# Kernel optimization log

Measured on AMD Instinct MI355X. Metric: run time of the kernel, lower is better.

The kernel has to match this reference:

```python
import jax, jax.numpy as jnp
import numpy as np

# decoded layout constants
NN, NO, SD = 16, 8, 4          # num_neighbors, num_obstacles, state_dim_per_agent
B = 131072                      # batch rows
H1, E, HP, AD = 64, 16, 64, 2   # phi hidden, embed, psi hidden, action dim
D_ROBOT, D_OBST = 0.3, 0.3
B_GAMMA, B_EXPH = 0.05, 1.0
PHI_MIN, PHI_MAX = -2.0, 2.0
A_MAX = 2.0


def setup_inputs() -> dict:
    key = jax.random.key(0)
    kx, kw = jax.random.split(key)
    # x: [count | goal(SD) | NN neighbor rel-states (SD each) | NO obstacle rel-pos (2 each)]
    x = jax.random.normal(kx, (B, 1 + SD + SD * NN + 2 * NO), dtype=jnp.float32) * 2.0
    x = x.at[:, 0].set(float(NN))
    names = [("Wp1n", (SD, H1)), ("bp1n", (H1,)), ("Wp2n", (H1, E)), ("bp2n", (E,)),
             ("Wr1n", (E, H1)), ("br1n", (H1,)), ("Wr2n", (H1, E)), ("br2n", (E,)),
             ("Wp1o", (2, H1)), ("bp1o", (H1,)), ("Wp2o", (H1, E)), ("bp2o", (E,)),
             ("Wr1o", (E, H1)), ("br1o", (H1,)), ("Wr2o", (H1, E)), ("br2o", (E,)),
             ("Wpsi1", (2 * E + SD, HP)), ("bpsi1", (HP,)), ("Wpsi2", (HP, AD)), ("bpsi2", (AD,))]
    ks = jax.random.split(kw, len(names))
    inp = {"x": x}
    for (n, sh), k in zip(names, ks):
        s = 1.0 / np.sqrt(sh[0])  # torch Linear default init scale
        inp[n] = jax.random.uniform(k, sh, jnp.float32, -s, s)
    return inp


def _mlp2(h, W1, b1, W2, b2):
    # Feedforward: activation between layers, linear output
    return jax.nn.relu(h @ W1 + b1) @ W2 + b2


def _deepset(el, Wp1, bp1, Wp2, bp2, Wr1, br1, Wr2, br2):
    # el: [B, n, d] -> phi each element, sum over set, rho
    phi = _mlp2(el, Wp1, bp1, Wp2, bp2)          # [B, n, E]
    return _mlp2(phi.sum(axis=1), Wr1, br1, Wr2, br2)  # [B, E]


def _barrier_sum(P, D):
    # P: [B, n, 2]; APF barrier gamma * P / (|P| * (|P|-D)^exph), summed over n
    nrm = jnp.linalg.norm(P, axis=-1, keepdims=True)   # [B, n, 1]
    H = nrm - D
    return (B_GAMMA * P / (nrm * H ** B_EXPH)).sum(axis=1)  # [B, 2]


def reference(x, Wp1n, bp1n, Wp2n, bp2n, Wr1n, br1n, Wr2n, br2n,
              Wp1o, bp1o, Wp2o, bp2o, Wr1o, br1o, Wr2o, br2o,
              Wpsi1, bpsi1, Wpsi2, bpsi2):
    nb = x.shape[0]
    g = x[:, 1:1 + SD]                                        # goal
    nbr = x[:, 1 + SD:1 + SD + SD * NN].reshape(nb, NN, SD)   # neighbor rel-states
    obs = x[:, 1 + SD + SD * NN:].reshape(nb, NO, 2)          # obstacle rel-pos

    rho_n = _deepset(nbr, Wp1n, bp1n, Wp2n, bp2n, Wr1n, br1n, Wr2n, br2n)
    rho_o = _deepset(obs, Wp1o, bp1o, Wp2o, bp2o, Wr1o, br1o, Wr2o, br2o)

    h = jnp.concatenate([rho_n, rho_o, g], axis=1)            # [B, 2E+SD]
    emp = _mlp2(h, Wpsi1, bpsi1, Wpsi2, bpsi2)                # psi network
    emp = (jnp.tanh(emp) + 1.0) / 2.0 * (PHI_MAX - PHI_MIN) + PHI_MIN  # scale_empty

    bar = _barrier_sum(-nbr[:, :, :2], D_ROBOT) + _barrier_sum(-obs, D_OBST)

    action = emp + bar
    # scale(): divide rows whose inf-norm exceeds a_max
    inv_alpha = jnp.maximum(jnp.max(jnp.abs(action), axis=1, keepdims=True) / A_MAX, 1.0)
    return action / inv_alpha
```

## Files before the change

### kernel.cpp

```cpp
#include <hip/hip_runtime.h>
#include <math.h>


typedef __attribute__((ext_vector_type(8))) _Float16 f16x8;
typedef __attribute__((ext_vector_type(2))) __fp16 fp16x2;
typedef __attribute__((ext_vector_type(4))) float f32x4;

#define XW 85

#define FR_S1N  0
#define FR_S1O  4
#define FR_FN   8
#define FR_FO   16
#define FR_ZN   24
#define FR_ZO   32
#define FR_WG   40
#define FR_PSI2 44
#define FR_SPN  46
#define FR_SPO  50
#define N_FRAGS 54

#define BIG_STR 144
#define L_BIG  0
#define L_BIG2 2304
#define L_OUT  4608
#define L_BAR  4736
#define GRP_LDS 4864
#define NBA_STR 136

#define H16_ONE 0x00003C00u

__device__ __forceinline__ float fast_rcp(float x)  { return __builtin_amdgcn_rcpf(x); }
__device__ __forceinline__ float fast_sqrt(float x) { return __builtin_amdgcn_sqrtf(x); }

__device__ __forceinline__ float two_tanh(float a) {
    float ax = fabsf(a);
    float e = __expf(2.0f * ax);
    float t = 1.0f - 2.0f * fast_rcp(e + 1.0f);
    return copysignf(2.0f * t, a);
}

__device__ __forceinline__ void lds_order() {
    __asm__ __volatile__("" ::: "memory");
}

__device__ __forceinline__ unsigned pk2(float a, float b) {
    union { fp16x2 h; unsigned u; } t;
    t.h = __builtin_amdgcn_cvt_pkrtz(a, b);
    return t.u;
}
__device__ __forceinline__ f16x8 lds_af(const char* area, int stride, int off, int lane) {
    int mm = lane & 15, qq = lane >> 4;
    return *(const f16x8*)(area + mm * stride + off + qq * 16);
}
__device__ __forceinline__ f16x8 load_bh(const _Float16* wsf, int frag, int lane) {
    return ((const f16x8*)(wsf + (size_t)frag * 512))[lane];
}
__device__ __forceinline__ f32x4 cinit(float b) {
    f32x4 c; c[0] = b; c[1] = b; c[2] = b; c[3] = b; return c;
}
__device__ __forceinline__ f32x4 mfma1(f16x8 a, f16x8 b, f32x4 c) {
    return __builtin_amdgcn_mfma_f32_16x16x32_f16(a, b, c, 0, 0, 0);
}

__global__ void bn_prep(const float* __restrict__ Wp1n, const float* __restrict__ Wp2n,
                        const float* __restrict__ Wr1n, const float* __restrict__ Wr2n,
                        const float* __restrict__ Wp1o, const float* __restrict__ Wp2o,
                        const float* __restrict__ Wr1o, const float* __restrict__ Wr2o,
                        const float* __restrict__ Wpsi1, const float* __restrict__ Wpsi2,
                        const float* __restrict__ bp1n, const float* __restrict__ bp1o,
                        const float* __restrict__ bp2n, const float* __restrict__ bp2o,
                        const float* __restrict__ br1n, const float* __restrict__ br1o,
                        const float* __restrict__ br2n, const float* __restrict__ br2o,
                        const float* __restrict__ bpsi1,
                        _Float16* __restrict__ wsf)
{
    int f = blockIdx.x;
    int lane = threadIdx.x;
    int q = lane >> 4, c = lane & 15;

    if (f >= N_FRAGS) {
        float* dst = (float*)(wsf + (size_t)N_FRAGS * 512) + (f - N_FRAGS) * 64;
        if (lane < 64) {
            if (f == N_FRAGS) {
                float s = 0.f;
                for (int e = 0; e < 16; ++e) s = fmaf(bp2n[e], Wr1n[e * 64 + lane], s);
                dst[lane] = 16.f * s + br1n[lane];
            } else if (f == N_FRAGS + 1) {
                float s = 0.f;
                for (int e = 0; e < 16; ++e) s = fmaf(bp2o[e], Wr1o[e * 64 + lane], s);
                dst[lane] = 8.f * s + br1o[lane];
            } else if (f == N_FRAGS + 2) {
                dst[lane] = 16.f * bp1n[lane];
            } else {
                dst[lane] = 8.f * bp1o[lane];
            }
        }
        return;
    }

    _Float16* dstf = wsf + (size_t)f * 512 + lane * 8;

    if (f < 8) {
        const float* W   = (f < 4) ? Wp1n : Wp1o;
        const float* bia = (f < 4) ? bp1n : bp1o;
        int K  = (f < 4) ? 4 : 2;
        int nt = f & 3;
        for (int j = 0; j < 8; ++j) {
            int k = q * 8 + j;
            int n = nt * 16 + c;
            float v = 0.f;
            if (k < K) v = W[k * 64 + n];
            else if (k == K) v = bia[n];
            dstf[j] = (_Float16)v;
        }
    } else if (f < 24) {
        int rel = (f - 8) & 7;
        bool isN = f < 16;
        const float* Wa = isN ? Wp2n : Wp2o;
        const float* Wb = isN ? Wr1n : Wr1o;
        int kk = rel >> 2, nt = rel & 3;
        for (int j = 0; j < 8; ++j) {
            int k = kk * 32 + q * 8 + j;
            int n = nt * 16 + c;
            float s = 0.f;
            for (int e = 0; e < 16; ++e) s = fmaf(Wa[k * 16 + e], Wb[e * 64 + n], s);
            dstf[j] = (_Float16)(0.5f * s);
        }
    } else if (f < 40) {
        int rel = (f - 24) & 7;
        bool isN = f < 32;
        const float* Wa = isN ? Wr2n : Wr2o;
        int roff = isN ? 0 : 16;
        int kk = rel >> 2, nt = rel & 3;
        for (int j = 0; j < 8; ++j) {
            int k = kk * 32 + q * 8 + j;
            int n = nt * 16 + c;
            float s = 0.f;
            for (int e = 0; e < 16; ++e) s = fmaf(Wa[k * 16 + e], Wpsi1[(roff + e) * 64 + n], s);
            dstf[j] = (_Float16)s;
        }
    } else if (f < 44) {
        int nt = f - 40;
        for (int j = 0; j < 8; ++j) {
            int k = q * 8 + j;
            int n = nt * 16 + c;
            float v = 0.f;
            if (k < 4) v = Wpsi1[(32 + k) * 64 + n];
            else if (k == 4) {
                float s = bpsi1[n];
                for (int e = 0; e < 16; ++e) {
                    s = fmaf(br2n[e], Wpsi1[e * 64 + n], s);
                    s = fmaf(br2o[e], Wpsi1[(16 + e) * 64 + n], s);
                }
                v = s;
            }
            dstf[j] = (_Float16)v;
        }
    } else if (f < 46) {
        int kk = f - 44;
        for (int j = 0; j < 8; ++j) {
            int k = kk * 32 + q * 8 + j;
            float v = (c < 2) ? Wpsi2[k * 2 + c] : 0.f;
            dstf[j] = (_Float16)v;
        }
    } else if (f < 50) {
        int nt = f - 46;
        for (int j = 0; j < 8; ++j) {
            int k = q * 8 + j;
            int n = nt * 16 + c;
            dstf[j] = (_Float16)Wp1n[(k & 3) * 64 + n];
        }
    } else {
        int nt = f - 50;
        for (int j = 0; j < 8; ++j) {
            int k = q * 8 + j;
            int n = nt * 16 + c;
            float v = (k < 16) ? Wp1o[(k & 1) * 64 + n] : 0.f;
            dstf[j] = (_Float16)v;
        }
    }
}

__global__ __launch_bounds__(256, 4) void bn_main(
    const float* __restrict__ x, const _Float16* __restrict__ wsf,
    const float* __restrict__ bpsi2,
    float* __restrict__ out, int nb)
{
    __shared__ char smem[8 * GRP_LDS];
    const int lane = threadIdx.x & 63;
    const int wid  = threadIdx.x >> 6;
    const int g0   = blockIdx.x * 8 + wid * 2;
    const int row0 = g0 * 16;
    const int row1 = row0 + 16;

    char* Gl0  = smem + (wid * 2) * GRP_LDS;
    char* Gl1  = Gl0 + GRP_LDS;
    char* BIG0 = Gl0 + L_BIG;   char* BIG1 = Gl1 + L_BIG;
    char* BG20 = Gl0 + L_BIG2;  char* BG21 = Gl1 + L_BIG2;
    char* OUT0 = Gl0 + L_OUT;   char* OUT1 = Gl1 + L_OUT;
    char* BAR0 = Gl0 + L_BAR;   char* BAR1 = Gl1 + L_BAR;
    char* NBA0 = BIG0;          char* NBA1 = BIG1;

    const int m = lane & 15, q = lane >> 4, c = m;
    const float* xg0   = x + (size_t)row0 * XW;
    const float* xg1   = x + (size_t)row1 * XW;
    const float* xrow0 = xg0 + (size_t)m * XW;
    const float* xrow1 = xg1 + (size_t)m * XW;

    const float* BFN = (const float*)(wsf + (size_t)N_FRAGS * 512);
    const float* BFO = BFN + 64;

    const f32x4 ZC = cinit(0.f);

    {
        int ln5 = lane >> 5;
        int pr  = lane & 31;
        int mm0 = pr >> 1, fp = pr & 1;
        int dbo = mm0 * NBA_STR + fp * 4;
        const float* s00 = xg0 + (size_t)ln5 * XW + 5 + pr * 2;
        const float* s10 = xg1 + (size_t)ln5 * XW + 5 + pr * 2;
        #pragma unroll
        for (int t = 0; t < 8; ++t) {
            const float* sa = s00 + (size_t)(2 * t) * XW;
            const float* sb = s10 + (size_t)(2 * t) * XW;
            *(unsigned*)(NBA0 + dbo + (2 * t + ln5) * 8) = pk2(sa[0], sa[1]);
            *(unsigned*)(NBA1 + dbo + (2 * t + ln5) * 8) = pk2(sb[0], sb[1]);
        }
    }

    union { f16x8 v; unsigned u[4]; } gA0, gA1;
    gA0.u[0] = pk2(xrow0[1], xrow0[2]);
    gA0.u[1] = pk2(xrow0[3], xrow0[4]);
    gA0.u[2] = H16_ONE; gA0.u[3] = 0;
    gA1.u[0] = pk2(xrow1[1], xrow1[2]);
    gA1.u[1] = pk2(xrow1[3], xrow1[4]);
    gA1.u[2] = H16_ONE; gA1.u[3] = 0;

    unsigned obs0[8], obs1[8];
    #pragma unroll
    for (int t = 0; t < 8; ++t) {
        obs0[t] = pk2(xrow0[69 + 2 * t], xrow0[70 + 2 * t]);
        obs1[t] = pk2(xrow1[69 + 2 * t], xrow1[70 + 2 * t]);
    }

    {
        float bx0 = 0.f, by0 = 0.f, bx1 = 0.f, by1 = 0.f;
        #pragma unroll
        for (int i = 0; i < 4; ++i) {
            int n = 4 * q + i;
            float p0x = -xrow0[5 + 4 * n], p0y = -xrow0[6 + 4 * n];
            float n0 = fast_sqrt(p0x * p0x + p0y * p0y);
            float c0 = 0.05f * fast_rcp(n0 * (n0 - 0.3f));
            bx0 = fmaf(c0, p0x, bx0); by0 = fmaf(c0, p0y, by0);
            float p1x = -xrow1[5 + 4 * n], p1y = -xrow1[6 + 4 * n];
            float n1 = fast_sqrt(p1x * p1x + p1y * p1y);
            float c1 = 0.05f * fast_rcp(n1 * (n1 - 0.3f));
            bx1 = fmaf(c1, p1x, bx1); by1 = fmaf(c1, p1y, by1);
        }
        #pragma unroll
        for (int i = 0; i < 2; ++i) {
            int o = 2 * q + i;
            float p0x = -xrow0[69 + 2 * o], p0y = -xrow0[70 + 2 * o];
            float n0 = fast_sqrt(p0x * p0x + p0y * p0y);
            float c0 = 0.05f * fast_rcp(n0 * (n0 - 0.3f));
            bx0 = fmaf(c0, p0x, bx0); by0 = fmaf(c0, p0y, by0);
            float p1x = -xrow1[69 + 2 * o], p1y = -xrow1[70 + 2 * o];
            float n1 = fast_sqrt(p1x * p1x + p1y * p1y);
            float c1 = 0.05f * fast_rcp(n1 * (n1 - 0.3f));
            bx1 = fmaf(c1, p1x, bx1); by1 = fmaf(c1, p1y, by1);
        }
        bx0 += __shfl_xor(bx0, 16); by0 += __shfl_xor(by0, 16);
        bx0 += __shfl_xor(bx0, 32); by0 += __shfl_xor(by0, 32);
        bx1 += __shfl_xor(bx1, 16); by1 += __shfl_xor(by1, 16);
        bx1 += __shfl_xor(bx1, 32); by1 += __shfl_xor(by1, 32);
        if (q == 0) {
            float2 b0; b0.x = bx0; b0.y = by0; *(float2*)(BAR0 + m * 8) = b0;
            float2 b1; b1.x = bx1; b1.y = by1; *(float2*)(BAR1 + m * 8) = b1;
        }
    }

    {
        f16x8 Bs1o[4];
        #pragma unroll
        for (int nt = 0; nt < 4; ++nt) Bs1o[nt] = load_bh(wsf, FR_S1O + nt, lane);

        f32x4 aS0[4], aA0[4], aS1[4], aA1[4];
        #pragma unroll
        for (int nt = 0; nt < 4; ++nt) {
            aS0[nt] = cinit(0.f); aA0[nt] = cinit(0.f);
            aS1[nt] = cinit(0.f); aA1[nt] = cinit(0.f);
        }
        union { f16x8 v; unsigned u[4]; } A0, A1;
        A0.u[1] = H16_ONE; A0.u[2] = 0; A0.u[3] = 0;
        A1.u[1] = H16_ONE; A1.u[2] = 0; A1.u[3] = 0;
        #pragma unroll
        for (int oo = 0; oo < 8; ++oo) {
            A0.u[0] = obs0[oo];
            A1.u[0] = obs1[oo];
            #pragma unroll
            for (int nt = 0; nt < 4; ++nt) {
                aS0[nt] = mfma1(A0.v, Bs1o[nt], aS0[nt]);
                f32x4 c0 = mfma1(A0.v, Bs1o[nt], ZC);
                aS1[nt] = mfma1(A1.v, Bs1o[nt], aS1[nt]);
                f32x4 c1 = mfma1(A1.v, Bs1o[nt], ZC);
                #pragma unroll
                for (int reg = 0; reg < 4; ++reg) {
                    aA0[nt][reg] += fabsf(c0[reg]);
                    aA1[nt][reg] += fabsf(c1[reg]);
                }
            }
        }
        #pragma unroll
        for (int nt = 0; nt < 4; ++nt)
            #pragma unroll
            for (int reg = 0; reg < 4; ++reg) {
                *(_Float16*)(BG20 + (q * 4 + reg) * BIG_STR + (nt * 16 + c) * 2)
                    = (_Float16)(aS0[nt][reg] + aA0[nt][reg]);
                *(_Float16*)(BG21 + (q * 4 + reg) * BIG_STR + (nt * 16 + c) * 2)
                    = (_Float16)(aS1[nt][reg] + aA1[nt][reg]);
            }
    }
    lds_order();

    {
        f16x8 Bs1n[4];
        #pragma unroll
        for (int nt = 0; nt < 4; ++nt) Bs1n[nt] = load_bh(wsf, FR_S1N + nt, lane);

        const int m8 = m * 8;
        f32x4 aS0[4], aA0[4], aS1[4], aA1[4];
        #pragma unroll
        for (int nt = 0; nt < 4; ++nt) {
            aS0[nt] = cinit(0.f); aA0[nt] = cinit(0.f);
            aS1[nt] = cinit(0.f); aA1[nt] = cinit(0.f);
        }
        union { f16x8 v; unsigned u[4]; uint2 h[2]; } A0, A1;
        A0.u[2] = H16_ONE; A0.u[3] = 0;
        A1.u[2] = H16_ONE; A1.u[3] = 0;
        #pragma unroll
        for (int mm = 0; mm < 16; ++mm) {
            A0.h[0] = *(const uint2*)(NBA0 + mm * NBA_STR + m8);
            A1.h[0] = *(const uint2*)(NBA1 + mm * NBA_STR + m8);
            #pragma unroll
            for (int nt = 0; nt < 4; ++nt) {
                aS0[nt] = mfma1(A0.v, Bs1n[nt], aS0[nt]);
                f32x4 c0 = mfma1(A0.v, Bs1n[nt], ZC);
                aS1[nt] = mfma1(A1.v, Bs1n[nt], aS1[nt]);
                f32x4 c1 = mfma1(A1.v, Bs1n[nt], ZC);
                #pragma unroll
                for (int reg = 0; reg < 4; ++reg) {
                    aA0[nt][reg] += fabsf(c0[reg]);
                    aA1[nt][reg] += fabsf(c1[reg]);
                }
            }
        }
        lds_order();
        #pragma unroll
        for (int nt = 0; nt < 4; ++nt)
            #pragma unroll
            for (int reg = 0; reg < 4; ++reg) {
                *(_Float16*)(BIG0 + (q * 4 + reg) * BIG_STR + (nt * 16 + c) * 2)
                    = (_Float16)(aS0[nt][reg] + aA0[nt][reg]);
                *(_Float16*)(BIG1 + (q * 4 + reg) * BIG_STR + (nt * 16 + c) * 2)
                    = (_Float16)(aS1[nt][reg] + aA1[nt][reg]);
            }
    }
    lds_order();

    {
        f16x8 An00 = lds_af(BIG0, BIG_STR, 0, lane);
        f16x8 An01 = lds_af(BIG0, BIG_STR, 64, lane);
        f16x8 Ao00 = lds_af(BG20, BIG_STR, 0, lane);
        f16x8 Ao01 = lds_af(BG20, BIG_STR, 64, lane);
        f16x8 An10 = lds_af(BIG1, BIG_STR, 0, lane);
        f16x8 An11 = lds_af(BIG1, BIG_STR, 64, lane);
        f16x8 Ao10 = lds_af(BG21, BIG_STR, 0, lane);
        f16x8 Ao11 = lds_af(BG21, BIG_STR, 64, lane);
        #pragma unroll
        for (int nt = 0; nt < 4; ++nt) {
            f16x8 Bn0 = load_bh(wsf, FR_FN + nt, lane);
            f16x8 Bn1 = load_bh(wsf, FR_FN + 4 + nt, lane);
            f16x8 Bo0 = load_bh(wsf, FR_FO + nt, lane);
            f16x8 Bo1 = load_bh(wsf, FR_FO + 4 + nt, lane);
            float bfn = BFN[nt * 16 + c], bfo = BFO[nt * 16 + c];
            f32x4 cn0 = mfma1(An01, Bn1, mfma1(An00, Bn0, cinit(bfn)));
            f32x4 co0 = mfma1(Ao01, Bo1, mfma1(Ao00, Bo0, cinit(bfo)));
            f32x4 cn1 = mfma1(An11, Bn1, mfma1(An10, Bn0, cinit(bfn)));
            f32x4 co1 = mfma1(Ao11, Bo1, mfma1(Ao10, Bo0, cinit(bfo)));
            #pragma unroll
            for (int reg = 0; reg < 4; ++reg) {
                int off = (q * 4 + reg) * BIG_STR + (nt * 16 + c) * 2;
                *(_Float16*)(BIG0 + off) = (_Float16)fmaxf(cn0[reg], 0.f);
                *(_Float16*)(BG20 + off) = (_Float16)fmaxf(co0[reg], 0.f);
                *(_Float16*)(BIG1 + off) = (_Float16)fmaxf(cn1[reg], 0.f);
                *(_Float16*)(BG21 + off) = (_Float16)fmaxf(co1[reg], 0.f);
            }
        }
    }
    lds_order();

    {
        f16x8 An00 = lds_af(BIG0, BIG_STR, 0, lane);
        f16x8 An01 = lds_af(BIG0, BIG_STR, 64, lane);
        f16x8 Ao00 = lds_af(BG20, BIG_STR, 0, lane);
        f16x8 Ao01 = lds_af(BG20, BIG_STR, 64, lane);
        f16x8 An10 = lds_af(BIG1, BIG_STR, 0, lane);
        f16x8 An11 = lds_af(BIG1, BIG_STR, 64, lane);
        f16x8 Ao10 = lds_af(BG21, BIG_STR, 0, lane);
        f16x8 Ao11 = lds_af(BG21, BIG_STR, 64, lane);
        #pragma unroll
        for (int nt = 0; nt < 4; ++nt) {
            f16x8 Bg  = load_bh(wsf, FR_WG + nt, lane);
            f16x8 Bn0 = load_bh(wsf, FR_ZN + nt, lane);
            f16x8 Bn1 = load_bh(wsf, FR_ZN + 4 + nt, lane);
            f16x8 Bo0 = load_bh(wsf, FR_ZO + nt, lane);
            f16x8 Bo1 = load_bh(wsf, FR_ZO + 4 + nt, lane);
            f32x4 c0 = mfma1(gA0.v, Bg, ZC);
            c0 = mfma1(An00, Bn0, c0);
            c0 = mfma1(An01, Bn1, c0);
            c0 = mfma1(Ao00, Bo0, c0);
            c0 = mfma1(Ao01, Bo1, c0);
            f32x4 c1 = mfma1(gA1.v, Bg, ZC);
            c1 = mfma1(An10, Bn0, c1);
            c1 = mfma1(An11, Bn1, c1);
            c1 = mfma1(Ao10, Bo0, c1);
            c1 = mfma1(Ao11, Bo1, c1);
            #pragma unroll
            for (int reg = 0; reg < 4; ++reg) {
                int off = (q * 4 + reg) * BIG_STR + (nt * 16 + c) * 2;
                *(_Float16*)(BIG0 + off) = (_Float16)fmaxf(c0[reg], 0.f);
                *(_Float16*)(BIG1 + off) = (_Float16)fmaxf(c1[reg], 0.f);
            }
        }
    }
    lds_order();

    {
        float b_p2 = (c < 2) ? bpsi2[c] : 0.f;
        f16x8 Bp20 = load_bh(wsf, FR_PSI2 + 0, lane);
        f16x8 Bp21 = load_bh(wsf, FR_PSI2 + 1, lane);
        f16x8 A00 = lds_af(BIG0, BIG_STR, 0, lane);
        f16x8 A01 = lds_af(BIG0, BIG_STR, 64, lane);
        f16x8 A10 = lds_af(BIG1, BIG_STR, 0, lane);
        f16x8 A11 = lds_af(BIG1, BIG_STR, 64, lane);
        f32x4 c0 = mfma1(A01, Bp21, mfma1(A00, Bp20, cinit(b_p2)));
        f32x4 c1 = mfma1(A11, Bp21, mfma1(A10, Bp20, cinit(b_p2)));
        if (c < 2) {
            #pragma unroll
            for (int reg = 0; reg < 4; ++reg) {
                *(float*)(OUT0 + (q * 4 + reg) * 8 + c * 4) = c0[reg];
                *(float*)(OUT1 + (q * 4 + reg) * 8 + c * 4) = c1[reg];
            }
        }
    }
    lds_order();

    if (lane < 16) {
        float2 a0 = *(const float2*)(OUT0 + lane * 8);
        float2 b0 = *(const float2*)(BAR0 + lane * 8);
        float u0 = two_tanh(a0.x) + b0.x;
        float v0 = two_tanh(a0.y) + b0.y;
        float ia0 = fmaxf(fmaxf(fabsf(u0), fabsf(v0)) * 0.5f, 1.0f);
        float r0 = fast_rcp(ia0);
        float2 o0; o0.x = u0 * r0; o0.y = v0 * r0;
        *(float2*)(out + (size_t)(row0 + lane) * 2) = o0;

        float2 a1 = *(const float2*)(OUT1 + lane * 8);
        float2 b1 = *(const float2*)(BAR1 + lane * 8);
        float u1 = two_tanh(a1.x) + b1.x;
        float v1 = two_tanh(a1.y) + b1.y;
        float ia1 = fmaxf(fmaxf(fabsf(u1), fabsf(v1)) * 0.5f, 1.0f);
        float r1 = fast_rcp(ia1);
        float2 o1; o1.x = u1 * r1; o1.y = v1 * r1;
        *(float2*)(out + (size_t)(row1 + lane) * 2) = o1;
    }
}

extern "C" void kernel_launch(void* const* d_in, const int* in_sizes, int n_in,
                              void* d_out, int out_size, void* d_ws, size_t ws_size,
                              hipStream_t stream) {
    const float* x     = (const float*)d_in[0];
    const float* Wp1n  = (const float*)d_in[1];
    const float* bp1n  = (const float*)d_in[2];
    const float* Wp2n  = (const float*)d_in[3];
    const float* bp2n  = (const float*)d_in[4];
    const float* Wr1n  = (const float*)d_in[5];
    const float* br1n  = (const float*)d_in[6];
    const float* Wr2n  = (const float*)d_in[7];
    const float* br2n  = (const float*)d_in[8];
    const float* Wp1o  = (const float*)d_in[9];
    const float* bp1o  = (const float*)d_in[10];
    const float* Wp2o  = (const float*)d_in[11];
    const float* bp2o  = (const float*)d_in[12];
    const float* Wr1o  = (const float*)d_in[13];
    const float* br1o  = (const float*)d_in[14];
    const float* Wr2o  = (const float*)d_in[15];
    const float* br2o  = (const float*)d_in[16];
    const float* Wpsi1 = (const float*)d_in[17];
    const float* bpsi1 = (const float*)d_in[18];
    const float* Wpsi2 = (const float*)d_in[19];
    const float* bpsi2 = (const float*)d_in[20];
    float* out = (float*)d_out;

    int nb = in_sizes[0] / XW;
    _Float16* wsf = (_Float16*)d_ws;

    bn_prep<<<N_FRAGS + 4, 64, 0, stream>>>(Wp1n, Wp2n, Wr1n, Wr2n,
                                            Wp1o, Wp2o, Wr1o, Wr2o,
                                            Wpsi1, Wpsi2,
                                            bp1n, bp1o, bp2n, bp2o,
                                            br1n, br1o, br2n, br2o,
                                            bpsi1, wsf);

    int groups = (nb + 15) / 16;
    int blocks = (groups + 7) / 8;
    bn_main<<<blocks, 256, 0, stream>>>(x, wsf, bpsi2, out, nb);
}
```

Before: 150.8 us.

## Compute linear part of set-sum relu with packed K-dim MFMAs instead of per-element accumulation

The phi layer-1 sum over set elements is split as relu(z) = (z + |z|)/2. Previously the linear term was accumulated with one MFMA per element. Now the linear sum is computed directly by packing several elements along the MFMA K dimension against replicated weight fragments (SPN/SPO) with the bias preloaded. This roughly halves the MFMA count in the hot loops and removes one set of accumulators. Launch bounds are also lowered from 4 to 3 waves per SIMD, which gives more register room but may reduce occupancy.

```diff
diff --git a/kernel.cpp b/kernel.cpp
--- a/kernel.cpp
+++ b/kernel.cpp
@@ -182,7 +182,7 @@
     }
 }
 
-__global__ __launch_bounds__(256, 4) void bn_main(
+__global__ __launch_bounds__(256, 3) void bn_main(
     const float* __restrict__ x, const _Float16* __restrict__ wsf,
     const float* __restrict__ bpsi2,
     float* __restrict__ out, int nb)
@@ -210,6 +210,8 @@
 
     const float* BFN = (const float*)(wsf + (size_t)N_FRAGS * 512);
     const float* BFO = BFN + 64;
+    const float* BSN = BFN + 128;
+    const float* BSO = BFN + 192;
 
     const f32x4 ZC = cinit(0.f);
 
@@ -281,15 +283,24 @@
     }
 
     {
-        f16x8 Bs1o[4];
-        #pragma unroll
-        for (int nt = 0; nt < 4; ++nt) Bs1o[nt] = load_bh(wsf, FR_S1O + nt, lane);
-
-        f32x4 aS0[4], aA0[4], aS1[4], aA1[4];
+        f16x8 Bspo[4], Bs1o[4];
         #pragma unroll
         for (int nt = 0; nt < 4; ++nt) {
-            aS0[nt] = cinit(0.f); aA0[nt] = cinit(0.f);
-            aS1[nt] = cinit(0.f); aA1[nt] = cinit(0.f);
+            Bspo[nt] = load_bh(wsf, FR_SPO + nt, lane);
+            Bs1o[nt] = load_bh(wsf, FR_S1O + nt, lane);
+        }
+        union { f16x8 v; unsigned u[4]; } Ap0, Ap1;
+        #pragma unroll
+        for (int j = 0; j < 4; ++j) {
+            Ap0.u[j] = q == 0 ? obs0[j] : (q == 1 ? obs0[4 + j] : 0u);
+            Ap1.u[j] = q == 0 ? obs1[j] : (q == 1 ? obs1[4 + j] : 0u);
+        }
+        f32x4 aT0[4], aT1[4];
+        #pragma unroll
+        for (int nt = 0; nt < 4; ++nt) {
+            float b = BSO[nt * 16 + c];
+            aT0[nt] = mfma1(Ap0.v, Bspo[nt], cinit(b));
+            aT1[nt] = mfma1(Ap1.v, Bspo[nt], cinit(b));
         }
         union { f16x8 v; unsigned u[4]; } A0, A1;
         A0.u[1] = H16_ONE; A0.u[2] = 0; A0.u[3] = 0;
@@ -300,14 +311,12 @@
             A1.u[0] = obs1[oo];
             #pragma unroll
             for (int nt = 0; nt < 4; ++nt) {
-                aS0[nt] = mfma1(A0.v, Bs1o[nt], aS0[nt]);
                 f32x4 c0 = mfma1(A0.v, Bs1o[nt], ZC);
-                aS1[nt] = mfma1(A1.v, Bs1o[nt], aS1[nt]);
                 f32x4 c1 = mfma1(A1.v, Bs1o[nt], ZC);
                 #pragma unroll
                 for (int reg = 0; reg < 4; ++reg) {
-                    aA0[nt][reg] += fabsf(c0[reg]);
-                    aA1[nt][reg] += fabsf(c1[reg]);
+                    aT0[nt][reg] += fabsf(c0[reg]);
+                    aT1[nt][reg] += fabsf(c1[reg]);
                 }
             }
         }
@@ -316,24 +325,38 @@
             #pragma unroll
             for (int reg = 0; reg < 4; ++reg) {
                 *(_Float16*)(BG20 + (q * 4 + reg) * BIG_STR + (nt * 16 + c) * 2)
-                    = (_Float16)(aS0[nt][reg] + aA0[nt][reg]);
+                    = (_Float16)aT0[nt][reg];
                 *(_Float16*)(BG21 + (q * 4 + reg) * BIG_STR + (nt * 16 + c) * 2)
-                    = (_Float16)(aS1[nt][reg] + aA1[nt][reg]);
+                    = (_Float16)aT1[nt][reg];
             }
     }
     lds_order();
 
     {
-        f16x8 Bs1n[4];
-        #pragma unroll
-        for (int nt = 0; nt < 4; ++nt) Bs1n[nt] = load_bh(wsf, FR_S1N + nt, lane);
-
+        f16x8 Bspn[4], Bs1n[4];
+        #pragma unroll
+        for (int nt = 0; nt < 4; ++nt) {
+            Bspn[nt] = load_bh(wsf, FR_SPN + nt, lane);
+            Bs1n[nt] = load_bh(wsf, FR_S1N + nt, lane);
+        }
         const int m8 = m * 8;
-        f32x4 aS0[4], aA0[4], aS1[4], aA1[4];
+        union { f16x8 v; uint2 h[2]; } P00, P01;
+        P00.h[0] = *(const uint2*)(NBA0 + (2 * q) * NBA_STR + m8);
+        P00.h[1] = *(const uint2*)(NBA0 + (2 * q + 1) * NBA_STR + m8);
+        P01.h[0] = *(const uint2*)(NBA0 + (2 * q + 8) * NBA_STR + m8);
+        P01.h[1] = *(const uint2*)(NBA0 + (2 * q + 9) * NBA_STR + m8);
+        union { f16x8 v; uint2 h[2]; } P10, P11;
+        P10.h[0] = *(const uint2*)(NBA1 + (2 * q) * NBA_STR + m8);
+        P10.h[1] = *(const uint2*)(NBA1 + (2 * q + 1) * NBA_STR + m8);
+        P11.h[0] = *(const uint2*)(NBA1 + (2 * q + 8) * NBA_STR + m8);
+        P11.h[1] = *(const uint2*)(NBA1 + (2 * q + 9) * NBA_STR + m8);
+
+        f32x4 aT0[4], aT1[4];
         #pragma unroll
         for (int nt = 0; nt < 4; ++nt) {
-            aS0[nt] = cinit(0.f); aA0[nt] = cinit(0.f);
-            aS1[nt] = cinit(0.f); aA1[nt] = cinit(0.f);
+            float b = BSN[nt * 16 + c];
+            aT0[nt] = mfma1(P01.v, Bspn[nt], mfma1(P00.v, Bspn[nt], cinit(b)));
+            aT1[nt] = mfma1(P11.v, Bspn[nt], mfma1(P10.v, Bspn[nt], cinit(b)));
         }
         union { f16x8 v; unsigned u[4]; uint2 h[2]; } A0, A1;
         A0.u[2] = H16_ONE; A0.u[3] = 0;
@@ -344,14 +367,12 @@
             A1.h[0] = *(const uint2*)(NBA1 + mm * NBA_STR + m8);
             #pragma unroll
             for (int nt = 0; nt < 4; ++nt) {
-                aS0[nt] = mfma1(A0.v, Bs1n[nt], aS0[nt]);
                 f32x4 c0 = mfma1(A0.v, Bs1n[nt], ZC);
-                aS1[nt] = mfma1(A1.v, Bs1n[nt], aS1[nt]);
                 f32x4 c1 = mfma1(A1.v, Bs1n[nt], ZC);
                 #pragma unroll
                 for (int reg = 0; reg < 4; ++reg) {
-                    aA0[nt][reg] += fabsf(c0[reg]);
-                    aA1[nt][reg] += fabsf(c1[reg]);
+                    aT0[nt][reg] += fabsf(c0[reg]);
+                    aT1[nt][reg] += fabsf(c1[reg]);
                 }
             }
         }
@@ -361,9 +382,9 @@
             #pragma unroll
             for (int reg = 0; reg < 4; ++reg) {
                 *(_Float16*)(BIG0 + (q * 4 + reg) * BIG_STR + (nt * 16 + c) * 2)
-                    = (_Float16)(aS0[nt][reg] + aA0[nt][reg]);
+                    = (_Float16)aT0[nt][reg];
                 *(_Float16*)(BIG1 + (q * 4 + reg) * BIG_STR + (nt * 16 + c) * 2)
-                    = (_Float16)(aS1[nt][reg] + aA1[nt][reg]);
+                    = (_Float16)aT1[nt][reg];
             }
     }
     lds_order();
```

Result: faster. 136.7 us (median of 2 runs) (-9.3%).
